# Performance work log

Measured on AMD Instinct MI355X. Metric: run time of the kernel, lower is better.

## Reference

```python
import jax, jax.numpy as jnp
import numpy as np

DIM_NODES = 128
DIM_EDGES = 64

def rms_norm(x, weight):
    eps = jnp.finfo(x.dtype).eps  # torch nn.RMSNorm default eps
    var = jnp.mean(jnp.square(x), axis=-1, keepdims=True)
    return x * jax.lax.rsqrt(var + eps) * weight

def setup_inputs() -> dict:
    key = jax.random.key(0)
    ks = jax.random.split(key, 6)
    B, N = 2, 512
    edges = jax.random.normal(ks[0], (B, N, N, DIM_EDGES), dtype=jnp.float32)
    nodes = jax.random.normal(ks[1], (B, N, DIM_NODES), dtype=jnp.float32)
    g_node = jnp.ones((DIM_NODES,), dtype=jnp.float32)
    g_edge = jnp.ones((DIM_EDGES,), dtype=jnp.float32)
    din = 2 * DIM_NODES + DIM_EDGES
    W = jax.random.normal(ks[2], (din, DIM_EDGES), dtype=jnp.float32) / np.sqrt(din)
    b = jax.random.normal(ks[3], (DIM_EDGES,), dtype=jnp.float32) * 0.01
    return {"edges": edges, "nodes": nodes, "g_node": g_node, "g_edge": g_edge, "W": W, "b": b}

def reference(edges, nodes, g_node, g_edge, W, b):
    # RMSNorms
    nodes_n = rms_norm(nodes, g_node)          # [B, N, dn]
    edges_n = rms_norm(edges, g_edge)          # [B, N, N, de]
    dn = nodes.shape[-1]
    # Decompose Linear over concat([rows, cols, edges]) into three matmuls
    # summed via broadcasting -- same math as cat+Linear, no O(N^2 * 2dn) blowup.
    Wr, Wc, We = W[:dn], W[dn:2 * dn], W[2 * dn:]
    row_proj = jnp.einsum('bid,de->bie', nodes_n, Wr)   # [B, N, de]
    col_proj = jnp.einsum('bjd,de->bje', nodes_n, Wc)   # [B, N, de]
    edge_proj = jnp.einsum('bijd,de->bije', edges_n, We)  # [B, N, N, de]
    out = edge_proj + row_proj[:, :, None, :] + col_proj[:, None, :, :] + b
    return out
```

## Files before the change

### kernel.cpp

```cpp
#include <hip/hip_runtime.h>
#include <hip/hip_bf16.h>

#define DN 128
#define DE 64
#define NN 512

typedef __bf16 bf16x8 __attribute__((ext_vector_type(8)));
typedef float  f32x4  __attribute__((ext_vector_type(4)));

__global__ void prep_nodes(const float* __restrict__ nodes,
                           const float* __restrict__ g_node,
                           const float* __restrict__ W,
                           const float* __restrict__ bias,
                           float* __restrict__ rp, float* __restrict__ cp) {
    const int row = blockIdx.x;
    const int l   = threadIdx.x;
    __shared__ float nn[DN];

    float x0 = nodes[row * DN + l];
    float x1 = nodes[row * DN + l + 64];
    float ssq = x0 * x0 + x1 * x1;
    #pragma unroll
    for (int m = 1; m < 64; m <<= 1) ssq += __shfl_xor(ssq, m, 64);
    float scale = rsqrtf(ssq * (1.0f / DN) + 1.1920929e-7f);
    nn[l]      = x0 * scale * g_node[l];
    nn[l + 64] = x1 * scale * g_node[l + 64];
    __syncthreads();

    float accr = bias[l];
    float accc = 0.0f;
    #pragma unroll 4
    for (int d = 0; d < DN; ++d) {
        float nd = nn[d];
        accr += nd * W[d * DE + l];
        accc += nd * W[(DN + d) * DE + l];
    }
    rp[row * DE + l] = accr;
    cp[row * DE + l] = accc;
}

__global__ void prep_weg(const float* __restrict__ W,
                         const float* __restrict__ g_edge,
                         __bf16* __restrict__ weg) {
    const int l = threadIdx.x;
    for (int kh = 0; kh < 2; ++kh)
        for (int ct = 0; ct < 4; ++ct) {
            const int f = kh * 4 + ct;
            #pragma unroll
            for (int e = 0; e < 8; ++e) {
                const int k   = kh * 32 + (l >> 4) * 8 + e;
                const int col = ct * 16 + (l & 15);
                weg[(f * 64 + l) * 8 + e] =
                    (__bf16)(g_edge[k] * W[(2 * DN + k) * DE + col]);
            }
        }
}

__global__ __launch_bounds__(256) void main_kernel(
    const float* __restrict__ edges, const float* __restrict__ rp,
    const float* __restrict__ cp, const __bf16* __restrict__ weg,
    float* __restrict__ out) {
    const int bid  = blockIdx.x;
    const int row  = bid >> 1;
    const int jblk = bid & 1;
    const int w    = threadIdx.x >> 6;
    const int l    = threadIdx.x & 63;
    const int jw   = jblk * 256 + w * 64;

    bf16x8 wf[8];
    #pragma unroll
    for (int f = 0; f < 8; ++f)
        wf[f] = *reinterpret_cast<const bf16x8*>(weg + (f * 64 + l) * 8);

    const int r16 = l & 15;
    const int kg  = l >> 4;
    float rpv[4];
    #pragma unroll
    for (int c = 0; c < 4; ++c) rpv[c] = rp[row * DE + c * 16 + r16];

    const int bN = (row / NN) * NN;

    for (int t = 0; t < 4; ++t) {
        const int jt = jw + t * 16;
        const float* ep = edges + ((size_t)row * NN + jt + r16) * DE + kg * 8;
        f32x4 x0a = *reinterpret_cast<const f32x4*>(ep);
        f32x4 x0b = *reinterpret_cast<const f32x4*>(ep + 4);
        f32x4 x1a = *reinterpret_cast<const f32x4*>(ep + 32);
        f32x4 x1b = *reinterpret_cast<const f32x4*>(ep + 36);

        float ssq = 0.0f;
        #pragma unroll
        for (int e = 0; e < 4; ++e)
            ssq += x0a[e] * x0a[e] + x0b[e] * x0b[e]
                 + x1a[e] * x1a[e] + x1b[e] * x1b[e];
        ssq += __shfl_xor(ssq, 16, 64);
        ssq += __shfl_xor(ssq, 32, 64);
        const float scale = rsqrtf(ssq * (1.0f / DE) + 1.1920929e-7f);

        bf16x8 a0, a1;
        #pragma unroll
        for (int e = 0; e < 4; ++e) {
            a0[e]     = (__bf16)x0a[e];
            a0[e + 4] = (__bf16)x0b[e];
            a1[e]     = (__bf16)x1a[e];
            a1[e + 4] = (__bf16)x1b[e];
        }

        f32x4 acc[4];
        #pragma unroll
        for (int c = 0; c < 4; ++c) {
            f32x4 z = {0.f, 0.f, 0.f, 0.f};
            z = __builtin_amdgcn_mfma_f32_16x16x32_bf16(a0, wf[c],     z, 0, 0, 0);
            z = __builtin_amdgcn_mfma_f32_16x16x32_bf16(a1, wf[4 + c], z, 0, 0, 0);
            acc[c] = z;
        }

        float sc[4];
        #pragma unroll
        for (int r = 0; r < 4; ++r) sc[r] = __shfl(scale, kg * 4 + r, 64);

        #pragma unroll
        for (int r = 0; r < 4; ++r) {
            const int j = jt + kg * 4 + r;
            const float* cprow = cp + (size_t)(bN + j) * DE;
            float* orow = out + ((size_t)row * NN + j) * DE;
            #pragma unroll
            for (int c = 0; c < 4; ++c) {
                const int col = c * 16 + r16;
                orow[col] = acc[c][r] * sc[r] + rpv[c] + cprow[col];
            }
        }
    }
}

extern "C" void kernel_launch(void* const* d_in, const int* in_sizes, int n_in,
                              void* d_out, int out_size, void* d_ws, size_t ws_size,
                              hipStream_t stream) {
    const float* edges  = (const float*)d_in[0];
    const float* nodes  = (const float*)d_in[1];
    const float* g_node = (const float*)d_in[2];
    const float* g_edge = (const float*)d_in[3];
    const float* W      = (const float*)d_in[4];
    const float* bias   = (const float*)d_in[5];
    float* out = (float*)d_out;

    float*  rp  = (float*)d_ws;
    float*  cp  = rp + 1024 * DE;
    __bf16* weg = (__bf16*)(cp + 1024 * DE);

    prep_nodes<<<dim3(1024), dim3(64), 0, stream>>>(nodes, g_node, W, bias, rp, cp);
    prep_weg<<<dim3(1), dim3(64), 0, stream>>>(W, g_edge, weg);
    main_kernel<<<dim3(2048), dim3(256), 0, stream>>>(edges, rp, cp, weg, out);
}
```

Measured before the change: 68.59 us.

## Transpose MFMA operands for vectorized stores and merge prep kernels

Swaps the A/B operands of the MFMA so each lane holds four consecutive output columns of one edge row. Output and cp loads/stores become 16-byte vector accesses, and the per-row scale needs no cross-lane shuffles. The two prep kernels are merged into one launch with an extra block that builds the bf16 weight fragments. The t-loop is also fully unrolled. Risk: the store pattern per wavefront changes and register pressure rises from the unroll.

```diff
diff --git a/kernel.cpp b/kernel.cpp
--- a/kernel.cpp
+++ b/kernel.cpp
@@ -8,13 +8,29 @@
 typedef __bf16 bf16x8 __attribute__((ext_vector_type(8)));
 typedef float  f32x4  __attribute__((ext_vector_type(4)));
 
-__global__ void prep_nodes(const float* __restrict__ nodes,
-                           const float* __restrict__ g_node,
-                           const float* __restrict__ W,
-                           const float* __restrict__ bias,
-                           float* __restrict__ rp, float* __restrict__ cp) {
+__global__ void prep_kernel(const float* __restrict__ nodes,
+                            const float* __restrict__ g_node,
+                            const float* __restrict__ g_edge,
+                            const float* __restrict__ W,
+                            const float* __restrict__ bias,
+                            float* __restrict__ rp, float* __restrict__ cp,
+                            __bf16* __restrict__ weg) {
+    const int l = threadIdx.x;
+    if (blockIdx.x == 1024) {
+        for (int kh = 0; kh < 2; ++kh)
+            for (int ct = 0; ct < 4; ++ct) {
+                const int f = kh * 4 + ct;
+                #pragma unroll
+                for (int e = 0; e < 8; ++e) {
+                    const int k   = kh * 32 + (l >> 4) * 8 + e;
+                    const int col = ct * 16 + (l & 15);
+                    weg[(f * 64 + l) * 8 + e] =
+                        (__bf16)(g_edge[k] * W[(2 * DN + k) * DE + col]);
+                }
+            }
+        return;
+    }
     const int row = blockIdx.x;
-    const int l   = threadIdx.x;
     __shared__ float nn[DN];
 
     float x0 = nodes[row * DN + l];
@@ -39,23 +55,6 @@
     cp[row * DE + l] = accc;
 }
 
-__global__ void prep_weg(const float* __restrict__ W,
-                         const float* __restrict__ g_edge,
-                         __bf16* __restrict__ weg) {
-    const int l = threadIdx.x;
-    for (int kh = 0; kh < 2; ++kh)
-        for (int ct = 0; ct < 4; ++ct) {
-            const int f = kh * 4 + ct;
-            #pragma unroll
-            for (int e = 0; e < 8; ++e) {
-                const int k   = kh * 32 + (l >> 4) * 8 + e;
-                const int col = ct * 16 + (l & 15);
-                weg[(f * 64 + l) * 8 + e] =
-                    (__bf16)(g_edge[k] * W[(2 * DN + k) * DE + col]);
-            }
-        }
-}
-
 __global__ __launch_bounds__(256) void main_kernel(
     const float* __restrict__ edges, const float* __restrict__ rp,
     const float* __restrict__ cp, const __bf16* __restrict__ weg,
@@ -74,15 +73,19 @@
 
     const int r16 = l & 15;
     const int kg  = l >> 4;
-    float rpv[4];
+
+    f32x4 rpv[4];
     #pragma unroll
-    for (int c = 0; c < 4; ++c) rpv[c] = rp[row * DE + c * 16 + r16];
+    for (int c = 0; c < 4; ++c)
+        rpv[c] = *reinterpret_cast<const f32x4*>(rp + row * DE + c * 16 + kg * 4);
 
     const int bN = (row / NN) * NN;
 
+    #pragma unroll
     for (int t = 0; t < 4; ++t) {
         const int jt = jw + t * 16;
-        const float* ep = edges + ((size_t)row * NN + jt + r16) * DE + kg * 8;
+        const int j  = jt + r16;
+        const float* ep = edges + ((size_t)row * NN + j) * DE + kg * 8;
         f32x4 x0a = *reinterpret_cast<const f32x4*>(ep);
         f32x4 x0b = *reinterpret_cast<const f32x4*>(ep + 4);
         f32x4 x1a = *reinterpret_cast<const f32x4*>(ep + 32);
@@ -106,29 +109,21 @@
             a1[e + 4] = (__bf16)x1b[e];
         }
 
-        f32x4 acc[4];
+        const float* cprow = cp  + (size_t)(bN + j) * DE + kg * 4;
+        float*       orow  = out + ((size_t)row * NN + j) * DE + kg * 4;
+
         #pragma unroll
         for (int c = 0; c < 4; ++c) {
             f32x4 z = {0.f, 0.f, 0.f, 0.f};
-            z = __builtin_amdgcn_mfma_f32_16x16x32_bf16(a0, wf[c],     z, 0, 0, 0);
-            z = __builtin_amdgcn_mfma_f32_16x16x32_bf16(a1, wf[4 + c], z, 0, 0, 0);
-            acc[c] = z;
-        }
+            z = __builtin_amdgcn_mfma_f32_16x16x32_bf16(wf[c],     a0, z, 0, 0, 0);
+            z = __builtin_amdgcn_mfma_f32_16x16x32_bf16(wf[4 + c], a1, z, 0, 0, 0);
 
-        float sc[4];
-        #pragma unroll
-        for (int r = 0; r < 4; ++r) sc[r] = __shfl(scale, kg * 4 + r, 64);
-
-        #pragma unroll
-        for (int r = 0; r < 4; ++r) {
-            const int j = jt + kg * 4 + r;
-            const float* cprow = cp + (size_t)(bN + j) * DE;
-            float* orow = out + ((size_t)row * NN + j) * DE;
+            f32x4 cp4 = *reinterpret_cast<const f32x4*>(cprow + c * 16);
+            f32x4 o;
             #pragma unroll
-            for (int c = 0; c < 4; ++c) {
-                const int col = c * 16 + r16;
-                orow[col] = acc[c][r] * sc[r] + rpv[c] + cprow[col];
-            }
+            for (int r = 0; r < 4; ++r)
+                o[r] = z[r] * scale + rpv[c][r] + cp4[r];
+            *reinterpret_cast<f32x4*>(orow + c * 16) = o;
         }
     }
 }
@@ -148,7 +143,7 @@
     float*  cp  = rp + 1024 * DE;
     __bf16* weg = (__bf16*)(cp + 1024 * DE);
 
-    prep_nodes<<<dim3(1024), dim3(64), 0, stream>>>(nodes, g_node, W, bias, rp, cp);
-    prep_weg<<<dim3(1), dim3(64), 0, stream>>>(W, g_edge, weg);
+    prep_kernel<<<dim3(1025), dim3(64), 0, stream>>>(nodes, g_node, g_edge, W,
+                                                     bias, rp, cp, weg);
     main_kernel<<<dim3(2048), dim3(256), 0, stream>>>(edges, rp, cp, weg, out);
 }
```

Result: slower. 71.15 us (+3.7%).
